# Performance work log

Measured on AMD Instinct MI355X. Metric: run time of the kernel, lower is better.

## Reference

```python
import jax, jax.numpy as jnp
import numpy as np

PI = np.pi
WIN = (8, 8)
N = WIN[0] * WIN[1]          # 64 tokens per window
NUM_HEADS = 8
DIM = 256
HEAD_DIM = DIM // NUM_HEADS  # 32
P = 4                        # Fourier series order (hardcoded in module)
W_RES = 64                   # input_resolution[1]
SCALE = HEAD_DIM ** -0.5
B_ = 1024                    # num_windows * batch


def _azimuth():
    # relative_coords[:, :, 1] from the torch module: relative column offsets
    ch = np.arange(WIN[0])
    cw = np.arange(WIN[1])
    gh, gw = np.meshgrid(ch, cw, indexing='ij')
    cf = np.stack([gh.ravel(), gw.ravel()])          # (2, N)
    rel = cf[:, :, None] - cf[:, None, :]            # (2, N, N)
    return jnp.asarray(rel[1], dtype=jnp.float32)    # (N, N)


def setup_inputs() -> dict:
    key = jax.random.key(0)
    ks = jax.random.split(key, 12)
    std = 0.02
    return {
        'x': jax.random.normal(ks[0], (B_, N, DIM), dtype=jnp.float32),
        'D': jax.random.uniform(ks[1], (B_, N), dtype=jnp.float32),
        'a_p': std * jax.random.normal(ks[2], (P + 1, NUM_HEADS), dtype=jnp.float32),
        'b_p': std * jax.random.normal(ks[3], (P, NUM_HEADS), dtype=jnp.float32),
        'a_r': std * jax.random.normal(ks[4], (P + 1, NUM_HEADS), dtype=jnp.float32),
        'b_r': std * jax.random.normal(ks[5], (P, NUM_HEADS), dtype=jnp.float32),
        'qkv_w': std * jax.random.normal(ks[6], (3 * DIM, DIM), dtype=jnp.float32),
        'qkv_b': jnp.zeros((3 * DIM,), dtype=jnp.float32),
        'proj_w': std * jax.random.normal(ks[7], (DIM, DIM), dtype=jnp.float32),
        'proj_b': jnp.zeros((DIM,), dtype=jnp.float32),
    }


def reference(x, D, a_p, b_p, a_r, b_r, qkv_w, qkv_b, proj_w, proj_b):
    B, n, C = x.shape

    # ---- azimuth Fourier bias: A_phi, shape (H, N, N) ----
    az = _azimuth() * (2.0 * PI / W_RES)                       # (N, N)
    ii = jnp.arange(1, P + 1, dtype=x.dtype)[:, None, None]    # (P, 1, 1)
    cosP = jnp.cos(ii * az)                                    # (P, N, N)
    sinP = jnp.sin(ii * az)
    A_phi = (jnp.einsum('ph,pij->hij', a_p[1:], cosP)
             + jnp.einsum('ph,pij->hij', b_p, sinP)) / P + a_p[0][:, None, None]

    # ---- radius Fourier bias: A_r, shape (B, N, N, H); rad[b,i,j] = D[b,j] - D[b,i] ----
    rad = D[:, None, :] - D[:, :, None]                        # (B, N, N)
    r_max = 2.0                                                # module overwrites r_max = 2
    A_r = jnp.zeros(rad.shape + (NUM_HEADS,), dtype=x.dtype)
    for i in range(1, P + 1):
        arg = rad * (2.0 * PI * i / r_max)
        A_r = A_r + jnp.cos(arg)[..., None] * a_r[i] + jnp.sin(arg)[..., None] * b_r[i - 1]
    A_r = A_r / P + a_r[0]                                     # (B, N, N, H)

    # ---- attention ----
    qkv = (x @ qkv_w.T + qkv_b).reshape(B, n, 3, NUM_HEADS, HEAD_DIM)
    qkv = qkv.transpose(2, 0, 3, 1, 4)                         # (3, B, H, N, hd)
    q, k, v = qkv[0], qkv[1], qkv[2]
    attn = jnp.einsum('bhid,bhjd->bhij', q * SCALE, k)
    attn = attn + A_phi[None] + A_r.transpose(0, 3, 1, 2)
    attn = jax.nn.softmax(attn, axis=-1)
    out = jnp.einsum('bhij,bhjd->bhid', attn, v)
    out = out.transpose(0, 2, 1, 3).reshape(B, n, C)
    return out @ proj_w.T + proj_b
```

## Files before the change

### kernel.cpp

```cpp
#include <hip/hip_runtime.h>
#include <hip/hip_bf16.h>


using short8  = __attribute__((ext_vector_type(8))) short;
using short4v = __attribute__((ext_vector_type(4))) short;
using floatx4 = __attribute__((ext_vector_type(4))) float;

#define PI_F    3.14159265358979323846f
#define SCALE_F 0.17677669529663687f

__device__ __forceinline__ short bfs(float x) {
  __hip_bfloat16 h = __float2bfloat16(x);
  return __builtin_bit_cast(short, h);
}

__global__ void prep_kernel(const float* __restrict__ qw,
                            const float* __restrict__ pw,
                            __hip_bfloat16* __restrict__ dst) {
  int g = blockIdx.x * 256 + threadIdx.x;
  const float4* src;
  __hip_bfloat16* d;
  if (g < 49152) { src = (const float4*)qw + g; d = dst + g * 4; }
  else { int g2 = g - 49152; src = (const float4*)pw + g2; d = dst + 196608 + g2 * 4; }
  float4 v = *src;
  d[0] = __float2bfloat16(v.x);
  d[1] = __float2bfloat16(v.y);
  d[2] = __float2bfloat16(v.z);
  d[3] = __float2bfloat16(v.w);
}

__device__ __forceinline__ void fourier_feats(float dv, int col, float* f) {
  float s1, c1; __sincosf(PI_F * dv, &s1, &c1);
  float c2 = c1*c1 - s1*s1, s2 = 2.f*s1*c1;
  float c3 = c2*c1 - s2*s1, s3 = s2*c1 + c2*s1;
  float c4 = c2*c2 - s2*s2, s4 = 2.f*s2*c2;
  float sa1, ca1; __sincosf((2.f * PI_F / 64.f) * (float)col, &sa1, &ca1);
  float ca2 = ca1*ca1 - sa1*sa1, sa2 = 2.f*sa1*ca1;
  float ca3 = ca2*ca1 - sa2*sa1, sa3 = sa2*ca1 + ca2*sa1;
  float ca4 = ca2*ca2 - sa2*sa2, sa4 = 2.f*sa2*ca2;
  f[0]=c1;  f[1]=c2;  f[2]=c3;  f[3]=c4;
  f[4]=s1;  f[5]=s2;  f[6]=s3;  f[7]=s4;
  f[8]=ca1; f[9]=ca2; f[10]=ca3; f[11]=ca4;
  f[12]=sa1; f[13]=sa2; f[14]=sa3; f[15]=sa4;
}

__global__ __launch_bounds__(1024, 4) void fused_kernel(
    const float* __restrict__ x, const float* __restrict__ D,
    const float* __restrict__ a_p, const float* __restrict__ b_p,
    const float* __restrict__ a_r, const float* __restrict__ b_r,
    const __hip_bfloat16* __restrict__ wq, const float* __restrict__ qkv_b,
    const __hip_bfloat16* __restrict__ pwb, const float* __restrict__ pb,
    float* __restrict__ out)
{
  constexpr int LDX = 264, LDQ = 264, LDK = 264, LDQf = 40, LDKm = 136,
                LDVt = 72, LDP = 68, LDO = 264;
  __shared__ __align__(16) __hip_bfloat16 sScr[17408];
  __shared__ __align__(16) __hip_bfloat16 sQ  [64 * 264];
  __shared__ __align__(16) __hip_bfloat16 sK  [64 * 264];
  __shared__ __align__(16) __hip_bfloat16 sQf [64 * 40];
  __shared__ __align__(16) __hip_bfloat16 sKm [64 * 136];
  __shared__ __align__(16) __hip_bfloat16 sVt [256 * 72];

  const int tid = threadIdx.x;
  const int lane = tid & 63, w = tid >> 6;
  const int laneN = lane & 15, laneQ = lane >> 4;
  const int b = blockIdx.x;
  const floatx4 fzero = {0.f, 0.f, 0.f, 0.f};
  const short8 zero8 = {0, 0, 0, 0, 0, 0, 0, 0};

  const float4* xg = (const float4*)(x + (size_t)b * 16384);
  #pragma unroll
  for (int it = 0; it < 4; ++it) {
    int g = tid + it * 1024;
    float4 v = xg[g];
    int t = g >> 6, c = (g & 63) * 4;
    short4v pk = { bfs(v.x), bfs(v.y), bfs(v.z), bfs(v.w) };
    *(short4v*)&sScr[t * LDX + c] = pk;
  }
  if (tid < 64) {
    float f[16];
    fourier_feats(D[b * 64 + tid], tid & 7, f);
    short8 q0, q1;
    #pragma unroll
    for (int i = 0; i < 8; ++i) { q0[i] = bfs(f[i]); q1[i] = bfs(f[8 + i]); }
    *(short8*)&sQf[tid * LDQf +  0] = q0;
    *(short8*)&sQf[tid * LDQf +  8] = q1;
    *(short8*)&sQf[tid * LDQf + 16] = zero8;
    *(short8*)&sQf[tid * LDQf + 24] = zero8;
  }
  if (tid < 512) {
    int t = tid >> 3, hh = tid & 7;
    float f[16];
    fourier_feats(D[b * 64 + t], t & 7, f);
    short8 v0, v1;
    #pragma unroll
    for (int p = 0; p < 4; ++p) {
      float ar = a_r[(p + 1) * 8 + hh], br = b_r[p * 8 + hh];
      float ap = a_p[(p + 1) * 8 + hh], bp = b_p[p * 8 + hh];
      float cr = f[p], sr = f[4 + p], ca = f[8 + p], sa = f[12 + p];
      v0[p]     = bfs((ar * cr + br * sr) * 0.25f);
      v0[4 + p] = bfs((ar * sr - br * cr) * 0.25f);
      v1[p]     = bfs((ap * ca - bp * sa) * 0.25f);
      v1[4 + p] = bfs((ap * sa + bp * ca) * 0.25f);
    }
    *(short8*)&sKm[t * LDKm + hh * 16 + 0] = v0;
    *(short8*)&sKm[t * LDKm + hh * 16 + 8] = v1;
  }
  __syncthreads();

  {
    const __hip_bfloat16* w0 = wq + (size_t)(      w * 16 + laneN) * 256;
    const __hip_bfloat16* w1 = wq + (size_t)(256 + w * 16 + laneN) * 256;
    const __hip_bfloat16* w2 = wq + (size_t)(512 + w * 16 + laneN) * 256;
    floatx4 accQ[4], accK[4], accV[4];
    #pragma unroll
    for (int mt = 0; mt < 4; ++mt) { accQ[mt] = fzero; accK[mt] = fzero; accV[mt] = fzero; }
    #pragma unroll
    for (int kk = 0; kk < 8; ++kk) {
      short8 a4[4];
      #pragma unroll
      for (int mt = 0; mt < 4; ++mt)
        a4[mt] = *(const short8*)&sScr[(mt * 16 + laneN) * LDX + kk * 32 + laneQ * 8];
      short8 b0 = *(const short8*)&w0[kk * 32 + laneQ * 8];
      short8 b1 = *(const short8*)&w1[kk * 32 + laneQ * 8];
      short8 b2 = *(const short8*)&w2[kk * 32 + laneQ * 8];
      #pragma unroll
      for (int mt = 0; mt < 4; ++mt) {
        accQ[mt] = __builtin_amdgcn_mfma_f32_16x16x32_bf16(b0, a4[mt], accQ[mt], 0, 0, 0);
        accK[mt] = __builtin_amdgcn_mfma_f32_16x16x32_bf16(b1, a4[mt], accK[mt], 0, 0, 0);
        accV[mt] = __builtin_amdgcn_mfma_f32_16x16x32_bf16(a4[mt], b2, accV[mt], 0, 0, 0);
      }
    }
    float4 bq4 = *(const float4*)&qkv_b[      w * 16 + laneQ * 4];
    float4 bk4 = *(const float4*)&qkv_b[256 + w * 16 + laneQ * 4];
    float bv   = qkv_b[512 + w * 16 + laneN];
    float bqa[4] = {bq4.x, bq4.y, bq4.z, bq4.w};
    float bka[4] = {bk4.x, bk4.y, bk4.z, bk4.w};
    #pragma unroll
    for (int mt = 0; mt < 4; ++mt) {
      short4v pq, pk, pv;
      #pragma unroll
      for (int r = 0; r < 4; ++r) {
        pq[r] = bfs((accQ[mt][r] + bqa[r]) * SCALE_F);
        pk[r] = bfs(accK[mt][r] + bka[r]);
        pv[r] = bfs(accV[mt][r] + bv);
      }
      *(short4v*)&sQ [(mt * 16 + laneN) * LDQ + w * 16 + laneQ * 4] = pq;
      *(short4v*)&sK [(mt * 16 + laneN) * LDK + w * 16 + laneQ * 4] = pk;
      *(short4v*)&sVt[(w * 16 + laneN) * LDVt + mt * 16 + laneQ * 4] = pv;
    }
  }
  __syncthreads();

  const int h = w >> 1, gm0 = (w & 1) * 2;
  short8 kf0[4], kf1[4];
  #pragma unroll
  for (int nt = 0; nt < 4; ++nt) {
    kf0[nt] = *(const short8*)&sK[(nt * 16 + laneN) * LDK + h * 32 + laneQ * 8];
    short8 km = *(const short8*)&sKm[(nt * 16 + laneN) * LDKm + h * 16 + (laneQ & 1) * 8];
    kf1[nt] = (laneQ < 2) ? km : zero8;
  }
  short8 vb[2][2];
  #pragma unroll
  for (int ont = 0; ont < 2; ++ont)
    #pragma unroll
    for (int kk = 0; kk < 2; ++kk)
      vb[ont][kk] = *(const short8*)&sVt[(h * 32 + ont * 16 + laneN) * LDVt + kk * 32 + laneQ * 8];

  floatx4 oacc[2][2];
  __hip_bfloat16* Pw = &sScr[w * 16 * LDP];
  #pragma unroll
  for (int m = 0; m < 2; ++m) {
    const int gm = gm0 + m;
    short8 q0 = *(const short8*)&sQ [(gm * 16 + laneN) * LDQ + h * 32 + laneQ * 8];
    short8 q1 = *(const short8*)&sQf[(gm * 16 + laneN) * LDQf + laneQ * 8];
    floatx4 s[4];
    #pragma unroll
    for (int nt = 0; nt < 4; ++nt) {
      s[nt] = __builtin_amdgcn_mfma_f32_16x16x32_bf16(q0, kf0[nt], fzero, 0, 0, 0);
      s[nt] = __builtin_amdgcn_mfma_f32_16x16x32_bf16(q1, kf1[nt], s[nt], 0, 0, 0);
    }
    #pragma unroll
    for (int r = 0; r < 4; ++r) {
      float mx = fmaxf(fmaxf(s[0][r], s[1][r]), fmaxf(s[2][r], s[3][r]));
      mx = fmaxf(mx, __shfl_xor(mx, 1));
      mx = fmaxf(mx, __shfl_xor(mx, 2));
      mx = fmaxf(mx, __shfl_xor(mx, 4));
      mx = fmaxf(mx, __shfl_xor(mx, 8));
      float e0 = __expf(s[0][r] - mx), e1 = __expf(s[1][r] - mx);
      float e2 = __expf(s[2][r] - mx), e3 = __expf(s[3][r] - mx);
      float sum = e0 + e1 + e2 + e3;
      sum += __shfl_xor(sum, 1);
      sum += __shfl_xor(sum, 2);
      sum += __shfl_xor(sum, 4);
      sum += __shfl_xor(sum, 8);
      float inv = __builtin_amdgcn_rcpf(sum);
      int pr = laneQ * 4 + r;
      Pw[pr * LDP +  0 + laneN] = __float2bfloat16(e0 * inv);
      Pw[pr * LDP + 16 + laneN] = __float2bfloat16(e1 * inv);
      Pw[pr * LDP + 32 + laneN] = __float2bfloat16(e2 * inv);
      Pw[pr * LDP + 48 + laneN] = __float2bfloat16(e3 * inv);
    }
    short4v p0a = *(const short4v*)&Pw[laneN * LDP + laneQ * 8];
    short4v p0b = *(const short4v*)&Pw[laneN * LDP + laneQ * 8 + 4];
    short4v p1a = *(const short4v*)&Pw[laneN * LDP + 32 + laneQ * 8];
    short4v p1b = *(const short4v*)&Pw[laneN * LDP + 36 + laneQ * 8];
    short8 pf0 = __builtin_shufflevector(p0a, p0b, 0, 1, 2, 3, 4, 5, 6, 7);
    short8 pf1 = __builtin_shufflevector(p1a, p1b, 0, 1, 2, 3, 4, 5, 6, 7);
    #pragma unroll
    for (int ont = 0; ont < 2; ++ont) {
      oacc[m][ont] = __builtin_amdgcn_mfma_f32_16x16x32_bf16(vb[ont][0], pf0, fzero, 0, 0, 0);
      oacc[m][ont] = __builtin_amdgcn_mfma_f32_16x16x32_bf16(vb[ont][1], pf1, oacc[m][ont], 0, 0, 0);
    }
  }
  __syncthreads();

  #pragma unroll
  for (int m = 0; m < 2; ++m)
    #pragma unroll
    for (int ont = 0; ont < 2; ++ont) {
      short4v pk;
      #pragma unroll
      for (int r = 0; r < 4; ++r) pk[r] = bfs(oacc[m][ont][r]);
      *(short4v*)&sScr[((gm0 + m) * 16 + laneN) * LDO + h * 32 + ont * 16 + laneQ * 4] = pk;
    }
  __syncthreads();

  const int col0 = w * 16;
  floatx4 pacc[4] = {fzero, fzero, fzero, fzero};
  const __hip_bfloat16* prow = pwb + (size_t)(col0 + laneN) * 256;
  #pragma unroll
  for (int kk = 0; kk < 8; ++kk) {
    short8 pbf = *(const short8*)&prow[kk * 32 + laneQ * 8];
    #pragma unroll
    for (int mt = 0; mt < 4; ++mt) {
      short8 pa = *(const short8*)&sScr[(mt * 16 + laneN) * LDO + kk * 32 + laneQ * 8];
      pacc[mt] = __builtin_amdgcn_mfma_f32_16x16x32_bf16(pbf, pa, pacc[mt], 0, 0, 0);
    }
  }
  float4 bias4 = *(const float4*)&pb[col0 + laneQ * 4];
  float* og = out + (size_t)b * 16384;
  #pragma unroll
  for (int mt = 0; mt < 4; ++mt) {
    float4 o4;
    o4.x = pacc[mt][0] + bias4.x;
    o4.y = pacc[mt][1] + bias4.y;
    o4.z = pacc[mt][2] + bias4.z;
    o4.w = pacc[mt][3] + bias4.w;
    *(float4*)&og[(mt * 16 + laneN) * 256 + col0 + laneQ * 4] = o4;
  }
}

extern "C" void kernel_launch(void* const* d_in, const int* in_sizes, int n_in,
                              void* d_out, int out_size, void* d_ws, size_t ws_size,
                              hipStream_t stream) {
  const float* x      = (const float*)d_in[0];
  const float* D      = (const float*)d_in[1];
  const float* a_p    = (const float*)d_in[2];
  const float* b_p    = (const float*)d_in[3];
  const float* a_r    = (const float*)d_in[4];
  const float* b_r    = (const float*)d_in[5];
  const float* qkv_w  = (const float*)d_in[6];
  const float* qkv_b  = (const float*)d_in[7];
  const float* proj_w = (const float*)d_in[8];
  const float* proj_b = (const float*)d_in[9];

  __hip_bfloat16* wq  = (__hip_bfloat16*)d_ws;
  __hip_bfloat16* pwb = wq + 196608;
  float* out = (float*)d_out;

  prep_kernel<<<256, 256, 0, stream>>>(qkv_w, proj_w, wq);
  fused_kernel<<<1024, 1024, 0, stream>>>(x, D, a_p, b_p, a_r, b_r, wq, qkv_b,
                                          pwb, proj_b, out);
}
```

Baseline: 215.2 us.

## Split fused window kernel into per-head-pair QKV+attention and separate projection kernel

```diff
diff --git a/kernel.cpp b/kernel.cpp
--- a/kernel.cpp
+++ b/kernel.cpp
@@ -5,6 +5,7 @@
 using short8  = __attribute__((ext_vector_type(8))) short;
 using short4v = __attribute__((ext_vector_type(4))) short;
 using floatx4 = __attribute__((ext_vector_type(4))) float;
+using uint4v  = __attribute__((ext_vector_type(4))) unsigned int;
 
 #define PI_F    3.14159265358979323846f
 #define SCALE_F 0.17677669529663687f
@@ -14,19 +15,10 @@
   return __builtin_bit_cast(short, h);
 }
 
-__global__ void prep_kernel(const float* __restrict__ qw,
-                            const float* __restrict__ pw,
-                            __hip_bfloat16* __restrict__ dst) {
-  int g = blockIdx.x * 256 + threadIdx.x;
-  const float4* src;
-  __hip_bfloat16* d;
-  if (g < 49152) { src = (const float4*)qw + g; d = dst + g * 4; }
-  else { int g2 = g - 49152; src = (const float4*)pw + g2; d = dst + 196608 + g2 * 4; }
-  float4 v = *src;
-  d[0] = __float2bfloat16(v.x);
-  d[1] = __float2bfloat16(v.y);
-  d[2] = __float2bfloat16(v.z);
-  d[3] = __float2bfloat16(v.w);
+__device__ __forceinline__ unsigned pk2(float a, float b) {
+  unsigned lo = (unsigned short)bfs(a);
+  unsigned hi = (unsigned short)bfs(b);
+  return lo | (hi << 16);
 }
 
 __device__ __forceinline__ void fourier_feats(float dv, int col, float* f) {
@@ -44,141 +36,179 @@
   f[12]=sa1; f[13]=sa2; f[14]=sa3; f[15]=sa4;
 }
 
-__global__ __launch_bounds__(1024, 4) void fused_kernel(
-    const float* __restrict__ x, const float* __restrict__ D,
+__global__ void prep_kernel(const float* __restrict__ qw,
+                            const float* __restrict__ pw,
+                            const float* __restrict__ x,
+                            __hip_bfloat16* __restrict__ dstW,
+                            __hip_bfloat16* __restrict__ xb) {
+  int blk = blockIdx.x, tid = threadIdx.x;
+  if (blk < 256) {
+    int g = blk * 256 + tid;
+    const float4* src;
+    __hip_bfloat16* d;
+    if (g < 49152) { src = (const float4*)qw + g; d = dstW + g * 4; }
+    else { int g2 = g - 49152; src = (const float4*)pw + g2; d = dstW + 196608 + g2 * 4; }
+    float4 v = *src;
+    d[0] = __float2bfloat16(v.x); d[1] = __float2bfloat16(v.y);
+    d[2] = __float2bfloat16(v.z); d[3] = __float2bfloat16(v.w);
+  } else {
+    int g = (blk - 256) * 256 + tid;
+    float4 v = ((const float4*)x)[g];
+    __hip_bfloat16* d = xb + (size_t)g * 4;
+    d[0] = __float2bfloat16(v.x); d[1] = __float2bfloat16(v.y);
+    d[2] = __float2bfloat16(v.z); d[3] = __float2bfloat16(v.w);
+  }
+}
+
+__global__ __launch_bounds__(256) void qkvattn_kernel(
+    const __hip_bfloat16* __restrict__ xb, const float* __restrict__ D,
     const float* __restrict__ a_p, const float* __restrict__ b_p,
     const float* __restrict__ a_r, const float* __restrict__ b_r,
     const __hip_bfloat16* __restrict__ wq, const float* __restrict__ qkv_b,
-    const __hip_bfloat16* __restrict__ pwb, const float* __restrict__ pb,
-    float* __restrict__ out)
+    __hip_bfloat16* __restrict__ Og)
 {
-  constexpr int LDX = 264, LDQ = 264, LDK = 264, LDQf = 40, LDKm = 136,
-                LDVt = 72, LDP = 68, LDO = 264;
-  __shared__ __align__(16) __hip_bfloat16 sScr[17408];
-  __shared__ __align__(16) __hip_bfloat16 sQ  [64 * 264];
-  __shared__ __align__(16) __hip_bfloat16 sK  [64 * 264];
-  __shared__ __align__(16) __hip_bfloat16 sQf [64 * 40];
-  __shared__ __align__(16) __hip_bfloat16 sKm [64 * 136];
-  __shared__ __align__(16) __hip_bfloat16 sVt [256 * 72];
+  __shared__ __align__(16) __hip_bfloat16 sQ  [64 * 72];
+  __shared__ __align__(16) __hip_bfloat16 sK  [64 * 72];
+  __shared__ __align__(16) __hip_bfloat16 sVt [64 * 72];
+  __shared__ __align__(16) __hip_bfloat16 sFeat[5120];
 
   const int tid = threadIdx.x;
   const int lane = tid & 63, w = tid >> 6;
   const int laneN = lane & 15, laneQ = lane >> 4;
   const int b = blockIdx.x;
+  const int win = b >> 2, hp = (b & 3) * 2;
+  const int hl = w >> 1, half = w & 1, H = hp + hl;
   const floatx4 fzero = {0.f, 0.f, 0.f, 0.f};
   const short8 zero8 = {0, 0, 0, 0, 0, 0, 0, 0};
 
-  const float4* xg = (const float4*)(x + (size_t)b * 16384);
-  #pragma unroll
-  for (int it = 0; it < 4; ++it) {
-    int g = tid + it * 1024;
-    float4 v = xg[g];
-    int t = g >> 6, c = (g & 63) * 4;
-    short4v pk = { bfs(v.x), bfs(v.y), bfs(v.z), bfs(v.w) };
-    *(short4v*)&sScr[t * LDX + c] = pk;
-  }
+  char* qb = (char*)sQ;
+  char* kb = (char*)sK;
+  char* vtb = (char*)sVt;
+  char* fb = (char*)sFeat;
+
   if (tid < 64) {
     float f[16];
-    fourier_feats(D[b * 64 + tid], tid & 7, f);
-    short8 q0, q1;
-    #pragma unroll
-    for (int i = 0; i < 8; ++i) { q0[i] = bfs(f[i]); q1[i] = bfs(f[8 + i]); }
-    *(short8*)&sQf[tid * LDQf +  0] = q0;
-    *(short8*)&sQf[tid * LDQf +  8] = q1;
-    *(short8*)&sQf[tid * LDQf + 16] = zero8;
-    *(short8*)&sQf[tid * LDQf + 24] = zero8;
-  }
-  if (tid < 512) {
-    int t = tid >> 3, hh = tid & 7;
+    fourier_feats(D[win * 64 + tid], tid & 7, f);
+    uint4v q0 = { pk2(f[0],f[1]),  pk2(f[2],f[3]),  pk2(f[4],f[5]),   pk2(f[6],f[7]) };
+    uint4v q1 = { pk2(f[8],f[9]),  pk2(f[10],f[11]),pk2(f[12],f[13]), pk2(f[14],f[15]) };
+    uint4v zz = { 0u, 0u, 0u, 0u };
+    *(uint4v*)(fb + tid * 80 +  0) = q0;
+    *(uint4v*)(fb + tid * 80 + 16) = q1;
+    *(uint4v*)(fb + tid * 80 + 32) = zz;
+    *(uint4v*)(fb + tid * 80 + 48) = zz;
+  }
+  if (tid < 128) {
+    int t = tid >> 1, hh = hp + (tid & 1);
     float f[16];
-    fourier_feats(D[b * 64 + t], t & 7, f);
-    short8 v0, v1;
+    fourier_feats(D[win * 64 + t], t & 7, f);
+    float m0[4], m1[4], m2[4], m3[4];
     #pragma unroll
     for (int p = 0; p < 4; ++p) {
-      float ar = a_r[(p + 1) * 8 + hh], br = b_r[p * 8 + hh];
-      float ap = a_p[(p + 1) * 8 + hh], bp = b_p[p * 8 + hh];
-      float cr = f[p], sr = f[4 + p], ca = f[8 + p], sa = f[12 + p];
-      v0[p]     = bfs((ar * cr + br * sr) * 0.25f);
-      v0[4 + p] = bfs((ar * sr - br * cr) * 0.25f);
-      v1[p]     = bfs((ap * ca - bp * sa) * 0.25f);
-      v1[4 + p] = bfs((ap * sa + bp * ca) * 0.25f);
-    }
-    *(short8*)&sKm[t * LDKm + hh * 16 + 0] = v0;
-    *(short8*)&sKm[t * LDKm + hh * 16 + 8] = v1;
+      float ar = a_r[(p+1)*8 + hh], br = b_r[p*8 + hh];
+      float ap = a_p[(p+1)*8 + hh], bp = b_p[p*8 + hh];
+      m0[p] = (ar*f[p]    + br*f[4+p])  * 0.25f;
+      m1[p] = (ar*f[4+p]  - br*f[p])    * 0.25f;
+      m2[p] = (ap*f[8+p]  - bp*f[12+p]) * 0.25f;
+      m3[p] = (ap*f[12+p] + bp*f[8+p])  * 0.25f;
+    }
+    uint4v k0 = { pk2(m0[0],m0[1]), pk2(m0[2],m0[3]), pk2(m1[0],m1[1]), pk2(m1[2],m1[3]) };
+    uint4v k1 = { pk2(m2[0],m2[1]), pk2(m2[2],m2[3]), pk2(m3[0],m3[1]), pk2(m3[2],m3[3]) };
+    *(uint4v*)(fb + 5120 + t * 80 + (tid & 1) * 32 +  0) = k0;
+    *(uint4v*)(fb + 5120 + t * 80 + (tid & 1) * 32 + 16) = k1;
+  }
+
+  const int r0q = H * 32 + half * 16;
+  const __hip_bfloat16* xw  = xb + (size_t)win * 16384;
+  const __hip_bfloat16* wQp = wq + (size_t)(      r0q + laneN) * 256 + laneQ * 8;
+  const __hip_bfloat16* wKp = wq + (size_t)(256 + r0q + laneN) * 256 + laneQ * 8;
+  const __hip_bfloat16* wVp = wq + (size_t)(512 + r0q + laneN) * 256 + laneQ * 8;
+
+  floatx4 aQ[4], aK[4], aV[4];
+  #pragma unroll
+  for (int mt = 0; mt < 4; ++mt) { aQ[mt]=fzero; aK[mt]=fzero; aV[mt]=fzero; }
+
+  #pragma unroll
+  for (int kk = 0; kk < 8; ++kk) {
+    short8 a4[4];
+    #pragma unroll
+    for (int mt = 0; mt < 4; ++mt)
+      a4[mt] = *(const short8*)&xw[(mt*16 + laneN) * 256 + kk*32 + laneQ*8];
+    short8 bq = *(const short8*)(wQp + kk*32);
+    short8 bk = *(const short8*)(wKp + kk*32);
+    short8 bv = *(const short8*)(wVp + kk*32);
+    #pragma unroll
+    for (int mt = 0; mt < 4; ++mt) {
+      aQ[mt] = __builtin_amdgcn_mfma_f32_16x16x32_bf16(bq, a4[mt], aQ[mt], 0, 0, 0);
+      aK[mt] = __builtin_amdgcn_mfma_f32_16x16x32_bf16(bk, a4[mt], aK[mt], 0, 0, 0);
+      aV[mt] = __builtin_amdgcn_mfma_f32_16x16x32_bf16(a4[mt], bv, aV[mt], 0, 0, 0);
+    }
+  }
+
+  {
+    const int cQ = hl * 64 + half * 32 + laneQ * 8;
+    float4 b4 = *(const float4*)&qkv_b[r0q + laneQ * 4];
+    float ba[4] = {b4.x, b4.y, b4.z, b4.w};
+    #pragma unroll
+    for (int mt = 0; mt < 4; ++mt) {
+      short4v pq;
+      #pragma unroll
+      for (int r = 0; r < 4; ++r) pq[r] = bfs((aQ[mt][r] + ba[r]) * SCALE_F);
+      *(short4v*)(qb + (mt*16 + laneN) * 144 + cQ) = pq;
+    }
+  }
+  {
+    const int cK = hl * 64 + half * 32 + laneQ * 8;
+    float4 b4 = *(const float4*)&qkv_b[256 + r0q + laneQ * 4];
+    float ba[4] = {b4.x, b4.y, b4.z, b4.w};
+    #pragma unroll
+    for (int mt = 0; mt < 4; ++mt) {
+      short4v pk;
+      #pragma unroll
+      for (int r = 0; r < 4; ++r) pk[r] = bfs(aK[mt][r] + ba[r]);
+      *(short4v*)(kb + (mt*16 + laneN) * 144 + cK) = pk;
+    }
+  }
+  {
+    float bv = qkv_b[512 + r0q + laneN];
+    const int vrow = hl * 32 + half * 16 + laneN;
+    #pragma unroll
+    for (int mt = 0; mt < 4; ++mt) {
+      short4v pv;
+      #pragma unroll
+      for (int r = 0; r < 4; ++r) pv[r] = bfs(aV[mt][r] + bv);
+      *(short4v*)(vtb + vrow * 144 + mt*32 + laneQ*8) = pv;
+    }
   }
   __syncthreads();
 
-  {
-    const __hip_bfloat16* w0 = wq + (size_t)(      w * 16 + laneN) * 256;
-    const __hip_bfloat16* w1 = wq + (size_t)(256 + w * 16 + laneN) * 256;
-    const __hip_bfloat16* w2 = wq + (size_t)(512 + w * 16 + laneN) * 256;
-    floatx4 accQ[4], accK[4], accV[4];
-    #pragma unroll
-    for (int mt = 0; mt < 4; ++mt) { accQ[mt] = fzero; accK[mt] = fzero; accV[mt] = fzero; }
-    #pragma unroll
-    for (int kk = 0; kk < 8; ++kk) {
-      short8 a4[4];
-      #pragma unroll
-      for (int mt = 0; mt < 4; ++mt)
-        a4[mt] = *(const short8*)&sScr[(mt * 16 + laneN) * LDX + kk * 32 + laneQ * 8];
-      short8 b0 = *(const short8*)&w0[kk * 32 + laneQ * 8];
-      short8 b1 = *(const short8*)&w1[kk * 32 + laneQ * 8];
-      short8 b2 = *(const short8*)&w2[kk * 32 + laneQ * 8];
-      #pragma unroll
-      for (int mt = 0; mt < 4; ++mt) {
-        accQ[mt] = __builtin_amdgcn_mfma_f32_16x16x32_bf16(b0, a4[mt], accQ[mt], 0, 0, 0);
-        accK[mt] = __builtin_amdgcn_mfma_f32_16x16x32_bf16(b1, a4[mt], accK[mt], 0, 0, 0);
-        accV[mt] = __builtin_amdgcn_mfma_f32_16x16x32_bf16(a4[mt], b2, accV[mt], 0, 0, 0);
-      }
-    }
-    float4 bq4 = *(const float4*)&qkv_b[      w * 16 + laneQ * 4];
-    float4 bk4 = *(const float4*)&qkv_b[256 + w * 16 + laneQ * 4];
-    float bv   = qkv_b[512 + w * 16 + laneN];
-    float bqa[4] = {bq4.x, bq4.y, bq4.z, bq4.w};
-    float bka[4] = {bk4.x, bk4.y, bk4.z, bk4.w};
-    #pragma unroll
-    for (int mt = 0; mt < 4; ++mt) {
-      short4v pq, pk, pv;
-      #pragma unroll
-      for (int r = 0; r < 4; ++r) {
-        pq[r] = bfs((accQ[mt][r] + bqa[r]) * SCALE_F);
-        pk[r] = bfs(accK[mt][r] + bka[r]);
-        pv[r] = bfs(accV[mt][r] + bv);
-      }
-      *(short4v*)&sQ [(mt * 16 + laneN) * LDQ + w * 16 + laneQ * 4] = pq;
-      *(short4v*)&sK [(mt * 16 + laneN) * LDK + w * 16 + laneQ * 4] = pk;
-      *(short4v*)&sVt[(w * 16 + laneN) * LDVt + mt * 16 + laneQ * 4] = pv;
-    }
+  const int gm0 = (w & 1) * 2;
+  short8 kf0[4], kf1[4], vf[2][2], q0[2], qff[2];
+  #pragma unroll
+  for (int nt = 0; nt < 4; ++nt) {
+    kf0[nt] = *(const short8*)(kb + (nt*16 + laneN) * 144 + hl*64 + laneQ*16);
+    short8 t8 = *(const short8*)(fb + 5120 + (nt*16 + laneN) * 80 + hl*32 + (laneQ & 1) * 16);
+    kf1[nt] = (laneQ < 2) ? t8 : zero8;
+  }
+  #pragma unroll
+  for (int ont = 0; ont < 2; ++ont)
+    #pragma unroll
+    for (int kkb = 0; kkb < 2; ++kkb)
+      vf[ont][kkb] = *(const short8*)(vtb + (hl*32 + ont*16 + laneN) * 144 + kkb*64 + laneQ*16);
+  #pragma unroll
+  for (int m = 0; m < 2; ++m) {
+    q0[m]  = *(const short8*)(qb + ((gm0+m)*16 + laneN) * 144 + hl*64 + laneQ*16);
+    qff[m] = *(const short8*)(fb + ((gm0+m)*16 + laneN) * 80 + laneQ*16);
   }
   __syncthreads();
 
-  const int h = w >> 1, gm0 = (w & 1) * 2;
-  short8 kf0[4], kf1[4];
-  #pragma unroll
-  for (int nt = 0; nt < 4; ++nt) {
-    kf0[nt] = *(const short8*)&sK[(nt * 16 + laneN) * LDK + h * 32 + laneQ * 8];
-    short8 km = *(const short8*)&sKm[(nt * 16 + laneN) * LDKm + h * 16 + (laneQ & 1) * 8];
-    kf1[nt] = (laneQ < 2) ? km : zero8;
-  }
-  short8 vb[2][2];
-  #pragma unroll
-  for (int ont = 0; ont < 2; ++ont)
-    #pragma unroll
-    for (int kk = 0; kk < 2; ++kk)
-      vb[ont][kk] = *(const short8*)&sVt[(h * 32 + ont * 16 + laneN) * LDVt + kk * 32 + laneQ * 8];
-
-  floatx4 oacc[2][2];
-  __hip_bfloat16* Pw = &sScr[w * 16 * LDP];
+  char* Pw = fb + w * 2176;
   #pragma unroll
   for (int m = 0; m < 2; ++m) {
-    const int gm = gm0 + m;
-    short8 q0 = *(const short8*)&sQ [(gm * 16 + laneN) * LDQ + h * 32 + laneQ * 8];
-    short8 q1 = *(const short8*)&sQf[(gm * 16 + laneN) * LDQf + laneQ * 8];
     floatx4 s[4];
     #pragma unroll
     for (int nt = 0; nt < 4; ++nt) {
-      s[nt] = __builtin_amdgcn_mfma_f32_16x16x32_bf16(q0, kf0[nt], fzero, 0, 0, 0);
-      s[nt] = __builtin_amdgcn_mfma_f32_16x16x32_bf16(q1, kf1[nt], s[nt], 0, 0, 0);
+      s[nt] = __builtin_amdgcn_mfma_f32_16x16x32_bf16(q0[m], kf0[nt], fzero, 0, 0, 0);
+      s[nt] = __builtin_amdgcn_mfma_f32_16x16x32_bf16(qff[m], kf1[nt], s[nt], 0, 0, 0);
     }
     #pragma unroll
     for (int r = 0; r < 4; ++r) {
@@ -196,58 +226,86 @@
       sum += __shfl_xor(sum, 8);
       float inv = __builtin_amdgcn_rcpf(sum);
       int pr = laneQ * 4 + r;
-      Pw[pr * LDP +  0 + laneN] = __float2bfloat16(e0 * inv);
-      Pw[pr * LDP + 16 + laneN] = __float2bfloat16(e1 * inv);
-      Pw[pr * LDP + 32 + laneN] = __float2bfloat16(e2 * inv);
-      Pw[pr * LDP + 48 + laneN] = __float2bfloat16(e3 * inv);
-    }
-    short4v p0a = *(const short4v*)&Pw[laneN * LDP + laneQ * 8];
-    short4v p0b = *(const short4v*)&Pw[laneN * LDP + laneQ * 8 + 4];
-    short4v p1a = *(const short4v*)&Pw[laneN * LDP + 32 + laneQ * 8];
-    short4v p1b = *(const short4v*)&Pw[laneN * LDP + 36 + laneQ * 8];
+      *(__hip_bfloat16*)(Pw + pr*136 +  0 + laneN*2) = __float2bfloat16(e0 * inv);
+      *(__hip_bfloat16*)(Pw + pr*136 + 32 + laneN*2) = __float2bfloat16(e1 * inv);
+      *(__hip_bfloat16*)(Pw + pr*136 + 64 + laneN*2) = __float2bfloat16(e2 * inv);
+      *(__hip_bfloat16*)(Pw + pr*136 + 96 + laneN*2) = __float2bfloat16(e3 * inv);
+    }
+    short4v p0a = *(const short4v*)(Pw + laneN*136 + laneQ*16);
+    short4v p0b = *(const short4v*)(Pw + laneN*136 + laneQ*16 + 8);
+    short4v p1a = *(const short4v*)(Pw + laneN*136 + 64 + laneQ*16);
+    short4v p1b = *(const short4v*)(Pw + laneN*136 + 72 + laneQ*16);
     short8 pf0 = __builtin_shufflevector(p0a, p0b, 0, 1, 2, 3, 4, 5, 6, 7);
     short8 pf1 = __builtin_shufflevector(p1a, p1b, 0, 1, 2, 3, 4, 5, 6, 7);
     #pragma unroll
     for (int ont = 0; ont < 2; ++ont) {
-      oacc[m][ont] = __builtin_amdgcn_mfma_f32_16x16x32_bf16(vb[ont][0], pf0, fzero, 0, 0, 0);
-      oacc[m][ont] = __builtin_amdgcn_mfma_f32_16x16x32_bf16(vb[ont][1], pf1, oacc[m][ont], 0, 0, 0);
-    }
+      floatx4 oa;
+      oa = __builtin_amdgcn_mfma_f32_16x16x32_bf16(vf[ont][0], pf0, fzero, 0, 0, 0);
+      oa = __builtin_amdgcn_mfma_f32_16x16x32_bf16(vf[ont][1], pf1, oa, 0, 0, 0);
+      short4v po;
+      #pragma unroll
+      for (int r = 0; r < 4; ++r) po[r] = bfs(oa[r]);
+      *(short4v*)&Og[(size_t)win * 16384 + ((gm0+m)*16 + laneN) * 256
+                     + H*32 + ont*16 + laneQ*4] = po;
+    }
+  }
+}
+
+__global__ __launch_bounds__(512) void proj_kernel(
+    const __hip_bfloat16* __restrict__ Og,
+    const __hip_bfloat16* __restrict__ pwb, const float* __restrict__ pb,
+    float* __restrict__ out)
+{
+  constexpr int LDO = 264;
+  __shared__ __align__(16) __hip_bfloat16 sO[64 * LDO];
+
+  const int tid = threadIdx.x;
+  const int lane = tid & 63, w = tid >> 6;
+  const int laneN = lane & 15, laneQ = lane >> 4;
+  const int b = blockIdx.x;
+  const size_t base = (size_t)b * 16384;
+  const floatx4 fzero = {0.f, 0.f, 0.f, 0.f};
+
+  #pragma unroll
+  for (int it = 0; it < 4; ++it) {
+    int e = (tid + it * 512) * 8;
+    int t = e >> 8, c = e & 255;
+    *(short8*)&sO[t * LDO + c] = *(const short8*)&Og[base + e];
   }
   __syncthreads();
 
-  #pragma unroll
-  for (int m = 0; m < 2; ++m)
-    #pragma unroll
-    for (int ont = 0; ont < 2; ++ont) {
-      short4v pk;
-      #pragma unroll
-      for (int r = 0; r < 4; ++r) pk[r] = bfs(oacc[m][ont][r]);
-      *(short4v*)&sScr[((gm0 + m) * 16 + laneN) * LDO + h * 32 + ont * 16 + laneQ * 4] = pk;
-    }
-  __syncthreads();
-
-  const int col0 = w * 16;
-  floatx4 pacc[4] = {fzero, fzero, fzero, fzero};
-  const __hip_bfloat16* prow = pwb + (size_t)(col0 + laneN) * 256;
+  floatx4 pacc[4][2];
+  #pragma unroll
+  for (int mt = 0; mt < 4; ++mt) { pacc[mt][0] = fzero; pacc[mt][1] = fzero; }
   #pragma unroll
   for (int kk = 0; kk < 8; ++kk) {
-    short8 pbf = *(const short8*)&prow[kk * 32 + laneQ * 8];
-    #pragma unroll
-    for (int mt = 0; mt < 4; ++mt) {
-      short8 pa = *(const short8*)&sScr[(mt * 16 + laneN) * LDO + kk * 32 + laneQ * 8];
-      pacc[mt] = __builtin_amdgcn_mfma_f32_16x16x32_bf16(pbf, pa, pacc[mt], 0, 0, 0);
-    }
-  }
-  float4 bias4 = *(const float4*)&pb[col0 + laneQ * 4];
-  float* og = out + (size_t)b * 16384;
-  #pragma unroll
-  for (int mt = 0; mt < 4; ++mt) {
-    float4 o4;
-    o4.x = pacc[mt][0] + bias4.x;
-    o4.y = pacc[mt][1] + bias4.y;
-    o4.z = pacc[mt][2] + bias4.z;
-    o4.w = pacc[mt][3] + bias4.w;
-    *(float4*)&og[(mt * 16 + laneN) * 256 + col0 + laneQ * 4] = o4;
+    short8 pa[4], pbf[2];
+    #pragma unroll
+    for (int mt = 0; mt < 4; ++mt)
+      pa[mt] = *(const short8*)&sO[(mt * 16 + laneN) * LDO + kk * 32 + laneQ * 8];
+    #pragma unroll
+    for (int n2 = 0; n2 < 2; ++n2)
+      pbf[n2] = *(const short8*)&pwb[(size_t)(w * 32 + n2 * 16 + laneN) * 256 + kk * 32 + laneQ * 8];
+    #pragma unroll
+    for (int mt = 0; mt < 4; ++mt)
+      #pragma unroll
+      for (int n2 = 0; n2 < 2; ++n2)
+        pacc[mt][n2] = __builtin_amdgcn_mfma_f32_16x16x32_bf16(pbf[n2], pa[mt], pacc[mt][n2], 0, 0, 0);
+  }
+  float* og = out + base;
+  #pragma unroll
+  for (int n2 = 0; n2 < 2; ++n2) {
+    int col0 = w * 32 + n2 * 16;
+    float4 bias4 = *(const float4*)&pb[col0 + laneQ * 4];
+    #pragma unroll
+    for (int mt = 0; mt < 4; ++mt) {
+      float4 o4;
+      o4.x = pacc[mt][n2][0] + bias4.x;
+      o4.y = pacc[mt][n2][1] + bias4.y;
+      o4.z = pacc[mt][n2][2] + bias4.z;
+      o4.w = pacc[mt][n2][3] + bias4.w;
+      *(float4*)&og[(mt * 16 + laneN) * 256 + col0 + laneQ * 4] = o4;
+    }
   }
 }
 
@@ -267,9 +325,12 @@
 
   __hip_bfloat16* wq  = (__hip_bfloat16*)d_ws;
   __hip_bfloat16* pwb = wq + 196608;
+  __hip_bfloat16* xb  = (__hip_bfloat16*)((char*)d_ws + 524288);
+  __hip_bfloat16* Og  = xb + 16777216;
   float* out = (float*)d_out;
 
-  prep_kernel<<<256, 256, 0, stream>>>(qkv_w, proj_w, wq);
-  fused_kernel<<<1024, 1024, 0, stream>>>(x, D, a_p, b_p, a_r, b_r, wq, qkv_b,
-                                          pwb, proj_b, out);
-}
+  prep_kernel<<<16640, 256, 0, stream>>>(qkv_w, proj_w, x, wq, xb);
+  qkvattn_kernel<<<4096, 256, 0, stream>>>(xb, D, a_p, b_p, a_r, b_r,
+                                           wq, qkv_b, Og);
+  proj_kernel<<<1024, 512, 0, stream>>>(Og, pwb, proj_b, out);
+}
```

Measured after the change: 289.0 us. 1.34x slower.
